# Performance work log

Hardware: AMD Instinct MI355X
Metric: run time of the kernel (lower is better)

The kernel has to match this reference:

```python
import jax, jax.numpy as jnp
from jax import lax
import numpy as np

D_MODEL = 256
EXPAND = 2
D_INNER = D_MODEL * EXPAND
B, T = 8, 4096


def setup_inputs() -> dict:
    key = jax.random.key(0)
    ks = jax.random.split(key, 7)
    s_lin = 1.0 / np.sqrt(D_MODEL)
    s_gru_i = 1.0 / np.sqrt(D_MODEL)  # torch GRU init: U(-1/sqrt(hidden), 1/sqrt(hidden))
    x = jax.random.normal(ks[0], (B, T, D_MODEL), dtype=jnp.float32)
    W1 = jax.random.uniform(ks[1], (D_INNER, D_MODEL), jnp.float32, -s_lin, s_lin)
    b1 = jax.random.uniform(ks[2], (D_INNER,), jnp.float32, -s_lin, s_lin)
    W_ih = jax.random.uniform(ks[3], (3 * D_MODEL, D_INNER), jnp.float32, -s_gru_i, s_gru_i)
    b_ih = jax.random.uniform(ks[4], (3 * D_MODEL,), jnp.float32, -s_gru_i, s_gru_i)
    W_hh = jax.random.uniform(ks[5], (3 * D_MODEL, D_MODEL), jnp.float32, -s_gru_i, s_gru_i)
    b_hh = jax.random.uniform(ks[6], (3 * D_MODEL,), jnp.float32, -s_gru_i, s_gru_i)
    return {"x": x, "W1": W1, "b1": b1, "W_ih": W_ih, "b_ih": b_ih, "W_hh": W_hh, "b_hh": b_hh}


def reference(x, W1, b1, W_ih, b_ih, W_hh, b_hh):
    # Linear(d_model -> d_inner) + exact GELU (torch default)
    h = jax.nn.gelu(jnp.einsum('btd,id->bti', x, W1) + b1, approximate=False)  # [B,T,Di]
    Bb, Tt, _ = h.shape
    H = W_hh.shape[1]
    # Precompute input-side gate pre-activations for all timesteps (order: r, z, n)
    gx = jnp.einsum('bti,gi->btg', h, W_ih) + b_ih  # [B,T,3H]
    gx = jnp.moveaxis(gx, 1, 0)                     # [T,B,3H]

    def step(hprev, g):
        gh = hprev @ W_hh.T + b_hh                  # [B,3H]
        xr, xz, xn = jnp.split(g, 3, axis=-1)
        hr, hz, hn = jnp.split(gh, 3, axis=-1)
        r = jax.nn.sigmoid(xr + hr)
        z = jax.nn.sigmoid(xz + hz)
        n = jnp.tanh(xn + r * hn)
        hnew = (1.0 - z) * n + z * hprev
        return hnew, hnew

    h0 = jnp.zeros((Bb, H), dtype=x.dtype)
    _, out = lax.scan(step, h0, gx)                 # out: [T,B,H]
    return jnp.moveaxis(out, 0, 1)                  # [B,T,H]
```

## Files before the change

kernel.cpp:

```cpp
#include <hip/hip_runtime.h>
#include <hip/hip_fp16.h>
#include <hip/hip_bf16.h>

#define DM   256
#define DI   512
#define TG   768
#define TSEQ 4096
#define NB   8
#define MTOT (NB*TSEQ)

typedef _Float16 h2f  __attribute__((ext_vector_type(2)));
typedef _Float16 h8f  __attribute__((ext_vector_type(8)));

template<bool A_HALF, bool GELU_ACT>
__global__ __launch_bounds__(256) void gemm_bias(
    const void* __restrict__ Ap, const float* __restrict__ W,
    const float* __restrict__ bias, __half* __restrict__ C,
    int M, int N, int K)
{
  __shared__ float As[16][132];
  __shared__ float Ws[16][132];
  const int tid = threadIdx.x;
  const int tx = tid & 15, ty = tid >> 4;
  const int m0 = blockIdx.y * 128;
  const int n0 = blockIdx.x * 128;

  float acc[8][8] = {};

  for (int k0 = 0; k0 < K; k0 += 16) {
    if constexpr (A_HALF) {
      const __half* A = (const __half*)Ap;
      int r = tid >> 1, seg = (tid & 1) * 8;
      float4 raw = *(const float4*)(A + (size_t)(m0 + r) * K + k0 + seg);
      const __half* hv = (const __half*)&raw;
      #pragma unroll
      for (int q = 0; q < 8; q++) As[seg + q][r] = __half2float(hv[q]);
    } else {
      const float* A = (const float*)Ap;
      #pragma unroll
      for (int rep = 0; rep < 2; rep++) {
        int r = (tid >> 2) + rep * 64;
        int seg = (tid & 3) * 4;
        float4 v = *(const float4*)(A + (size_t)(m0 + r) * K + k0 + seg);
        As[seg + 0][r] = v.x; As[seg + 1][r] = v.y;
        As[seg + 2][r] = v.z; As[seg + 3][r] = v.w;
      }
    }
    #pragma unroll
    for (int rep = 0; rep < 2; rep++) {
      int r = (tid >> 2) + rep * 64;
      int seg = (tid & 3) * 4;
      float4 v = *(const float4*)(W + (size_t)(n0 + r) * K + k0 + seg);
      Ws[seg + 0][r] = v.x; Ws[seg + 1][r] = v.y;
      Ws[seg + 2][r] = v.z; Ws[seg + 3][r] = v.w;
    }
    __syncthreads();
    #pragma unroll
    for (int kk = 0; kk < 16; ++kk) {
      float a[8], b[8];
      *(float4*)&a[0] = *(const float4*)&As[kk][ty * 8];
      *(float4*)&a[4] = *(const float4*)&As[kk][ty * 8 + 4];
      *(float4*)&b[0] = *(const float4*)&Ws[kk][tx * 8];
      *(float4*)&b[4] = *(const float4*)&Ws[kk][tx * 8 + 4];
      #pragma unroll
      for (int i = 0; i < 8; i++)
        #pragma unroll
        for (int j = 0; j < 8; j++)
          acc[i][j] += a[i] * b[j];
    }
    __syncthreads();
  }

  #pragma unroll
  for (int i = 0; i < 8; i++) {
    int m = m0 + ty * 8 + i;
    #pragma unroll
    for (int j = 0; j < 8; j++) {
      int n = n0 + tx * 8 + j;
      float v = acc[i][j] + bias[n];
      if constexpr (GELU_ACT) {
        v = 0.5f * v * (1.0f + erff(v * 0.70710678118654752f));
      }
      C[(size_t)m * N + n] = __float2half(v);
    }
  }
}

__device__ __forceinline__ float dpp_xor1_add(float v) {
  int i = __builtin_bit_cast(int, v);
  int s = __builtin_amdgcn_update_dpp(i, i, 0xB1, 0xF, 0xF, true);
  return v + __builtin_bit_cast(float, s);
}

#define D3(i) h2f wr##i, wz##i, wn##i;
#define L3(i) { float2 f_;                                                     \
    f_ = *(const float2*)(rr + 2*(i)); wr##i[0]=(_Float16)f_.x; wr##i[1]=(_Float16)f_.y; \
    f_ = *(const float2*)(rz + 2*(i)); wz##i[0]=(_Float16)f_.x; wz##i[1]=(_Float16)f_.y; \
    f_ = *(const float2*)(rn + 2*(i)); wn##i[0]=(_Float16)f_.x; wn##i[1]=(_Float16)f_.y; }

#define REP64(M) \
  M(0)  M(1)  M(2)  M(3)  M(4)  M(5)  M(6)  M(7)  \
  M(8)  M(9)  M(10) M(11) M(12) M(13) M(14) M(15) \
  M(16) M(17) M(18) M(19) M(20) M(21) M(22) M(23) \
  M(24) M(25) M(26) M(27) M(28) M(29) M(30) M(31) \
  M(32) M(33) M(34) M(35) M(36) M(37) M(38) M(39) \
  M(40) M(41) M(42) M(43) M(44) M(45) M(46) M(47) \
  M(48) M(49) M(50) M(51) M(52) M(53) M(54) M(55) \
  M(56) M(57) M(58) M(59) M(60) M(61) M(62) M(63)

#define REP64B4(M)  \
  M(0)  M(1)  M(2)  M(3)  SB M(4)  M(5)  M(6)  M(7)  SB \
  M(8)  M(9)  M(10) M(11) SB M(12) M(13) M(14) M(15) SB \
  M(16) M(17) M(18) M(19) SB M(20) M(21) M(22) M(23) SB \
  M(24) M(25) M(26) M(27) SB M(28) M(29) M(30) M(31) SB \
  M(32) M(33) M(34) M(35) SB M(36) M(37) M(38) M(39) SB \
  M(40) M(41) M(42) M(43) SB M(44) M(45) M(46) M(47) SB \
  M(48) M(49) M(50) M(51) SB M(52) M(53) M(54) M(55) SB \
  M(56) M(57) M(58) M(59) SB M(60) M(61) M(62) M(63) SB
#define SB __builtin_amdgcn_sched_barrier(0);

#define DSTEP(B, I0, I1, I2, I3) {                                        \
    h8f hh_ = hp[B];                                                      \
    h2f c0_ = __builtin_shufflevector(hh_, hh_, 0, 1);                    \
    h2f c1_ = __builtin_shufflevector(hh_, hh_, 2, 3);                    \
    h2f c2_ = __builtin_shufflevector(hh_, hh_, 4, 5);                    \
    h2f c3_ = __builtin_shufflevector(hh_, hh_, 6, 7);                    \
    ar0 = __builtin_amdgcn_fdot2(wr##I0, c0_, ar0, false);                \
    az0 = __builtin_amdgcn_fdot2(wz##I0, c0_, az0, false);                \
    an0 = __builtin_amdgcn_fdot2(wn##I0, c0_, an0, false);                \
    ar1 = __builtin_amdgcn_fdot2(wr##I1, c1_, ar1, false);                \
    az1 = __builtin_amdgcn_fdot2(wz##I1, c1_, az1, false);                \
    an1 = __builtin_amdgcn_fdot2(wn##I1, c1_, an1, false);                \
    ar0 = __builtin_amdgcn_fdot2(wr##I2, c2_, ar0, false);                \
    az0 = __builtin_amdgcn_fdot2(wz##I2, c2_, az0, false);                \
    an0 = __builtin_amdgcn_fdot2(wn##I2, c2_, an0, false);                \
    ar1 = __builtin_amdgcn_fdot2(wr##I3, c3_, ar1, false);                \
    az1 = __builtin_amdgcn_fdot2(wz##I3, c3_, az1, false);                \
    an1 = __builtin_amdgcn_fdot2(wn##I3, c3_, an1, false); }

__global__ __launch_bounds__(512, 1) __attribute__((amdgpu_waves_per_eu(2, 2)))
void gru_scan(
    const __half* __restrict__ gx,
    const float*  __restrict__ Whh,
    const float*  __restrict__ bhh,
    float* __restrict__ out)
{
  const int b = blockIdx.x;
  const int j = threadIdx.x;
  const int u = j >> 1;
  const int p = j & 1;

  __shared__ __align__(16) _Float16 hbuf[2][2][136];

  REP64(D3)
  {
    const float* rr = Whh + (size_t)u * DM + p * 128;
    const float* rz = rr + (size_t)DM * DM;
    const float* rn = rz + (size_t)DM * DM;
    REP64B4(L3)
  }
  const float br = bhh[u];
  const float bz = bhh[DM + u];
  const float bn = bhh[2 * DM + u];
  float hloc = 0.0f;

  if (j < DM) hbuf[0][j >> 7][j & 127] = (_Float16)0.0f;
  __syncthreads();

  const __half* gp = gx + (size_t)b * TSEQ * TG;
  float* outb = out + (size_t)b * TSEQ * DM;

  float gxr = __half2float(gp[u]);
  float gxz = __half2float(gp[DM + u]);
  float gxn = __half2float(gp[2 * DM + u]);

  for (int t = 0; t < TSEQ; ++t) {
    const int cur = t & 1;
    const h8f* hp = (const h8f*)(&hbuf[cur][p][0]);

    float nr = 0.f, nz = 0.f, nn = 0.f;
    if (t + 1 < TSEQ) {
      const __half* g1 = gp + TG;
      nr = __half2float(g1[u]);
      nz = __half2float(g1[DM + u]);
      nn = __half2float(g1[2 * DM + u]);
    }

    float ar0 = 0.f, ar1 = 0.f, az0 = 0.f, az1 = 0.f, an0 = 0.f, an1 = 0.f;
    DSTEP(0,  0,  1,  2,  3)  DSTEP(1,  4,  5,  6,  7)
    DSTEP(2,  8,  9,  10, 11) DSTEP(3,  12, 13, 14, 15)
    DSTEP(4,  16, 17, 18, 19) DSTEP(5,  20, 21, 22, 23)
    DSTEP(6,  24, 25, 26, 27) DSTEP(7,  28, 29, 30, 31)
    DSTEP(8,  32, 33, 34, 35) DSTEP(9,  36, 37, 38, 39)
    DSTEP(10, 40, 41, 42, 43) DSTEP(11, 44, 45, 46, 47)
    DSTEP(12, 48, 49, 50, 51) DSTEP(13, 52, 53, 54, 55)
    DSTEP(14, 56, 57, 58, 59) DSTEP(15, 60, 61, 62, 63)

    float ar = dpp_xor1_add(ar0 + ar1);
    float az = dpp_xor1_add(az0 + az1);
    float an = dpp_xor1_add(an0 + an1);

    float r = __builtin_amdgcn_rcpf(1.0f + __expf(-(gxr + ar + br)));
    float z = __builtin_amdgcn_rcpf(1.0f + __expf(-(gxz + az + bz)));
    float a = gxn + r * (an + bn);
    float e = __expf(-2.0f * __builtin_fabsf(a));
    float n = __builtin_copysignf((1.0f - e) * __builtin_amdgcn_rcpf(1.0f + e), a);
    float hnew = n + z * (hloc - n);
    hloc = hnew;

    if (p == 0) {
      hbuf[cur ^ 1][u >> 7][u & 127] = (_Float16)hnew;
      outb[(size_t)t * DM + u] = hnew;
    }
    __syncthreads();

    gp += TG;
    gxr = nr; gxz = nz; gxn = nn;
  }
}

extern "C" void kernel_launch(void* const* d_in, const int* in_sizes, int n_in,
                              void* d_out, int out_size, void* d_ws, size_t ws_size,
                              hipStream_t stream) {
  const float* x   = (const float*)d_in[0];
  const float* W1  = (const float*)d_in[1];
  const float* b1  = (const float*)d_in[2];
  const float* Wih = (const float*)d_in[3];
  const float* bih = (const float*)d_in[4];
  const float* Whh = (const float*)d_in[5];
  const float* bhh = (const float*)d_in[6];
  float* out = (float*)d_out;

  char* ws = (char*)d_ws;
  __half* h  = (__half*)ws;
  size_t h_bytes = (size_t)MTOT * DI * sizeof(__half);
  h_bytes = (h_bytes + 255) & ~(size_t)255;
  __half* gxbuf = (__half*)(ws + h_bytes);

  dim3 blk(256);
  gemm_bias<false, true><<<dim3(DI / 128, MTOT / 128), blk, 0, stream>>>(
      x, W1, b1, h, MTOT, DI, DM);
  gemm_bias<true, false><<<dim3(TG / 128, MTOT / 128), blk, 0, stream>>>(
      h, Wih, bih, gxbuf, MTOT, TG, DI);
  gru_scan<<<NB, 512, 0, stream>>>(gxbuf, Whh, bhh, out);
}
```

Measured before the change: 4.997 ms.

## Split GRU recurrent dot product across four lanes per hidden unit with 1024 threads

The GRU scan kernel now uses 1024 threads per batch block, with four lanes per hidden unit each handling 64 inputs instead of two lanes handling 128. Per-lane register weights are halved, and the partial sums are combined with two DPP reductions. Biases are folded into the accumulator initialisation, scaled by a quarter. This shortens the serial dot-product chain per timestep, at the cost of more waves contending for the per-step barrier and an extra cross-lane reduction.

```diff
diff --git a/kernel.cpp b/kernel.cpp
--- a/kernel.cpp
+++ b/kernel.cpp
@@ -1,6 +1,5 @@
 #include <hip/hip_runtime.h>
 #include <hip/hip_fp16.h>
-#include <hip/hip_bf16.h>
 
 #define DM   256
 #define DI   512
@@ -9,8 +8,8 @@
 #define NB   8
 #define MTOT (NB*TSEQ)
 
-typedef _Float16 h2f  __attribute__((ext_vector_type(2)));
-typedef _Float16 h8f  __attribute__((ext_vector_type(8)));
+typedef _Float16 h2f   __attribute__((ext_vector_type(2)));
+typedef _Float16 f16x8 __attribute__((ext_vector_type(8)));
 
 template<bool A_HALF, bool GELU_ACT>
 __global__ __launch_bounds__(256) void gemm_bias(
@@ -91,36 +90,26 @@
   int s = __builtin_amdgcn_update_dpp(i, i, 0xB1, 0xF, 0xF, true);
   return v + __builtin_bit_cast(float, s);
 }
-
-#define D3(i) h2f wr##i, wz##i, wn##i;
-#define L3(i) { float2 f_;                                                     \
+__device__ __forceinline__ float dpp_xor2_add(float v) {
+  int i = __builtin_bit_cast(int, v);
+  int s = __builtin_amdgcn_update_dpp(i, i, 0x4E, 0xF, 0xF, true);
+  return v + __builtin_bit_cast(float, s);
+}
+
+#define DW(i) h2f wr##i, wz##i, wn##i;
+#define LW(i) { float2 f_;                                                     \
     f_ = *(const float2*)(rr + 2*(i)); wr##i[0]=(_Float16)f_.x; wr##i[1]=(_Float16)f_.y; \
     f_ = *(const float2*)(rz + 2*(i)); wz##i[0]=(_Float16)f_.x; wz##i[1]=(_Float16)f_.y; \
     f_ = *(const float2*)(rn + 2*(i)); wn##i[0]=(_Float16)f_.x; wn##i[1]=(_Float16)f_.y; }
 
-#define REP64(M) \
+#define REP32(M) \
   M(0)  M(1)  M(2)  M(3)  M(4)  M(5)  M(6)  M(7)  \
   M(8)  M(9)  M(10) M(11) M(12) M(13) M(14) M(15) \
   M(16) M(17) M(18) M(19) M(20) M(21) M(22) M(23) \
-  M(24) M(25) M(26) M(27) M(28) M(29) M(30) M(31) \
-  M(32) M(33) M(34) M(35) M(36) M(37) M(38) M(39) \
-  M(40) M(41) M(42) M(43) M(44) M(45) M(46) M(47) \
-  M(48) M(49) M(50) M(51) M(52) M(53) M(54) M(55) \
-  M(56) M(57) M(58) M(59) M(60) M(61) M(62) M(63)
-
-#define REP64B4(M)  \
-  M(0)  M(1)  M(2)  M(3)  SB M(4)  M(5)  M(6)  M(7)  SB \
-  M(8)  M(9)  M(10) M(11) SB M(12) M(13) M(14) M(15) SB \
-  M(16) M(17) M(18) M(19) SB M(20) M(21) M(22) M(23) SB \
-  M(24) M(25) M(26) M(27) SB M(28) M(29) M(30) M(31) SB \
-  M(32) M(33) M(34) M(35) SB M(36) M(37) M(38) M(39) SB \
-  M(40) M(41) M(42) M(43) SB M(44) M(45) M(46) M(47) SB \
-  M(48) M(49) M(50) M(51) SB M(52) M(53) M(54) M(55) SB \
-  M(56) M(57) M(58) M(59) SB M(60) M(61) M(62) M(63) SB
-#define SB __builtin_amdgcn_sched_barrier(0);
+  M(24) M(25) M(26) M(27) M(28) M(29) M(30) M(31)
 
 #define DSTEP(B, I0, I1, I2, I3) {                                        \
-    h8f hh_ = hp[B];                                                      \
+    f16x8 hh_ = *(const f16x8*)(hp + (B) * 8);                            \
     h2f c0_ = __builtin_shufflevector(hh_, hh_, 0, 1);                    \
     h2f c1_ = __builtin_shufflevector(hh_, hh_, 2, 3);                    \
     h2f c2_ = __builtin_shufflevector(hh_, hh_, 4, 5);                    \
@@ -138,84 +127,74 @@
     az1 = __builtin_amdgcn_fdot2(wz##I3, c3_, az1, false);                \
     an1 = __builtin_amdgcn_fdot2(wn##I3, c3_, an1, false); }
 
-__global__ __launch_bounds__(512, 1) __attribute__((amdgpu_waves_per_eu(2, 2)))
+__global__ __launch_bounds__(1024, 1)
 void gru_scan(
     const __half* __restrict__ gx,
     const float*  __restrict__ Whh,
     const float*  __restrict__ bhh,
     float* __restrict__ out)
 {
-  const int b = blockIdx.x;
-  const int j = threadIdx.x;
-  const int u = j >> 1;
-  const int p = j & 1;
-
-  __shared__ __align__(16) _Float16 hbuf[2][2][136];
-
-  REP64(D3)
+  const int b   = blockIdx.x;
+  const int tid = threadIdx.x;
+  const int q   = tid >> 2;
+  const int p   = tid & 3;
+
+  __shared__ __align__(16) _Float16 hbuf[2][4][72];
+
+  REP32(DW)
   {
-    const float* rr = Whh + (size_t)u * DM + p * 128;
-    const float* rz = rr + (size_t)DM * DM;
-    const float* rn = rz + (size_t)DM * DM;
-    REP64B4(L3)
-  }
-  const float br = bhh[u];
-  const float bz = bhh[DM + u];
-  const float bn = bhh[2 * DM + u];
+    const float* rr = Whh + (size_t)q * DM + p * 64;
+    const float* rz = rr + 256 * DM;
+    const float* rn = rr + 512 * DM;
+    REP32(LW)
+  }
+  const float br4 = 0.25f * bhh[q];
+  const float bz4 = 0.25f * bhh[DM + q];
+  const float bn4 = 0.25f * bhh[2 * DM + q];
   float hloc = 0.0f;
 
-  if (j < DM) hbuf[0][j >> 7][j & 127] = (_Float16)0.0f;
+  if (tid < 2 * 4 * 72) ((_Float16*)hbuf)[tid] = (_Float16)0.0f;
   __syncthreads();
 
-  const __half* gp = gx + (size_t)b * TSEQ * TG;
-  float* outb = out + (size_t)b * TSEQ * DM;
-
-  float gxr = __half2float(gp[u]);
-  float gxz = __half2float(gp[DM + u]);
-  float gxn = __half2float(gp[2 * DM + u]);
+  const __half* g = gx + (size_t)b * TSEQ * TG + q;
+  float* outb = out + (size_t)b * TSEQ * DM + q;
+
+  __half grc = g[0], gzc = g[DM], gnc = g[2 * DM];
 
   for (int t = 0; t < TSEQ; ++t) {
-    const int cur = t & 1;
-    const h8f* hp = (const h8f*)(&hbuf[cur][p][0]);
-
-    float nr = 0.f, nz = 0.f, nn = 0.f;
-    if (t + 1 < TSEQ) {
-      const __half* g1 = gp + TG;
-      nr = __half2float(g1[u]);
-      nz = __half2float(g1[DM + u]);
-      nn = __half2float(g1[2 * DM + u]);
-    }
-
-    float ar0 = 0.f, ar1 = 0.f, az0 = 0.f, az1 = 0.f, an0 = 0.f, an1 = 0.f;
+    const int cur = t & 1, nxt = cur ^ 1;
+    const _Float16* hp = &hbuf[cur][p][0];
+
+    int tt = (t + 1 < TSEQ) ? t + 1 : t;
+    const __half* g1 = g + (size_t)tt * TG;
+    __half grn = g1[0], gzn = g1[DM], gnn = g1[2 * DM];
+
+    float ar0 = br4, ar1 = 0.f, az0 = bz4, az1 = 0.f, an0 = bn4, an1 = 0.f;
     DSTEP(0,  0,  1,  2,  3)  DSTEP(1,  4,  5,  6,  7)
-    DSTEP(2,  8,  9,  10, 11) DSTEP(3,  12, 13, 14, 15)
-    DSTEP(4,  16, 17, 18, 19) DSTEP(5,  20, 21, 22, 23)
-    DSTEP(6,  24, 25, 26, 27) DSTEP(7,  28, 29, 30, 31)
-    DSTEP(8,  32, 33, 34, 35) DSTEP(9,  36, 37, 38, 39)
-    DSTEP(10, 40, 41, 42, 43) DSTEP(11, 44, 45, 46, 47)
-    DSTEP(12, 48, 49, 50, 51) DSTEP(13, 52, 53, 54, 55)
-    DSTEP(14, 56, 57, 58, 59) DSTEP(15, 60, 61, 62, 63)
-
-    float ar = dpp_xor1_add(ar0 + ar1);
-    float az = dpp_xor1_add(az0 + az1);
-    float an = dpp_xor1_add(an0 + an1);
-
-    float r = __builtin_amdgcn_rcpf(1.0f + __expf(-(gxr + ar + br)));
-    float z = __builtin_amdgcn_rcpf(1.0f + __expf(-(gxz + az + bz)));
-    float a = gxn + r * (an + bn);
-    float e = __expf(-2.0f * __builtin_fabsf(a));
-    float n = __builtin_copysignf((1.0f - e) * __builtin_amdgcn_rcpf(1.0f + e), a);
-    float hnew = n + z * (hloc - n);
+    DSTEP(2,  8,  9, 10, 11)  DSTEP(3, 12, 13, 14, 15)
+    DSTEP(4, 16, 17, 18, 19)  DSTEP(5, 20, 21, 22, 23)
+    DSTEP(6, 24, 25, 26, 27)  DSTEP(7, 28, 29, 30, 31)
+
+    float ar = dpp_xor2_add(dpp_xor1_add(ar0 + ar1));
+    float az = dpp_xor2_add(dpp_xor1_add(az0 + az1));
+    float an = dpp_xor2_add(dpp_xor1_add(an0 + an1));
+
+    float xr = __half2float(grc), xz = __half2float(gzc), xn = __half2float(gnc);
+    float rg = __builtin_amdgcn_rcpf(1.0f + __expf(-(xr + ar)));
+    float zg = __builtin_amdgcn_rcpf(1.0f + __expf(-(xz + az)));
+    float ap = xn + rg * an;
+    float e  = __expf(-2.0f * __builtin_fabsf(ap));
+    float nn = __builtin_copysignf((1.0f - e) * __builtin_amdgcn_rcpf(1.0f + e), ap);
+    float hnew = nn + zg * (hloc - nn);
     hloc = hnew;
 
     if (p == 0) {
-      hbuf[cur ^ 1][u >> 7][u & 127] = (_Float16)hnew;
-      outb[(size_t)t * DM + u] = hnew;
+      hbuf[nxt][q >> 6][q & 63] = (_Float16)hnew;
+      outb[(size_t)t * DM] = hnew;
     }
     __syncthreads();
 
-    gp += TG;
-    gxr = nr; gxz = nz; gxn = nn;
+    grc = grn; gzc = gzn; gnc = gnn;
   }
 }
 
@@ -242,5 +221,5 @@
       x, W1, b1, h, MTOT, DI, DM);
   gemm_bias<true, false><<<dim3(TG / 128, MTOT / 128), blk, 0, stream>>>(
       h, Wih, bih, gxbuf, MTOT, TG, DI);
-  gru_scan<<<NB, 512, 0, stream>>>(gxbuf, Whh, bhh, out);
-}
+  gru_scan<<<NB, 1024, 0, stream>>>(gxbuf, Whh, bhh, out);
+}
```

New measurement: 5.603 ms. +12.1%, slower.
